# Kernel optimization log

Measured on AMD Instinct MI355X. Metric: run time of the kernel, lower is better.

## Reference

```python
import jax, jax.numpy as jnp
import numpy as np

EPS = 1e-32

def round_ste(x):
    # straight-through rounding: forward round, identity gradient
    return x + jax.lax.stop_gradient(jnp.round(x) - x)

def setup_inputs() -> dict:
    key = jax.random.key(0)
    x = jax.random.normal(key, (4096, 11008), dtype=jnp.float32)  # [out_ch, d_in]
    return {"x": x, "n_bits": 4}

def reference(x, n_bits):
    # --- find_params (per_channel=True, sym=True, method='log_2') ---
    half_levels = float(2 ** (n_bits - 1))  # number of log2 levels
    xmin = jnp.minimum(x.min(axis=1), 0.0)          # [C]
    xmax = jnp.maximum(x.max(axis=1), 0.0)          # [C]
    xmax = jnp.maximum(jnp.abs(xmin), xmax)         # symmetric range
    xmin = -xmax
    # get_code_map, branch code_no_2 >= 2^(n_bits-1): pure base-2 codes
    max_val = jnp.floor(jnp.log2(xmax + EPS) + 0.5)
    neg_max_val = jnp.floor(jnp.log2(-xmin + EPS) + 0.5)
    max_val = jnp.maximum(max_val, neg_max_val)
    zero = (max_val - half_levels + 1.0)[:, None]   # [C,1] zero point (min exponent)
    # asym_map = 0 (sym), code_map = all True -> real_code_map = 2, scale = 1 (p=1)
    # --- quantize (method='log_2', hardware_approx=False) ---
    x_log = jnp.log2(jnp.abs(x) + EPS)              # log(|x/scale|+eps)/log(2), scale=1
    x_int = round_ste(x_log)
    x_c1 = jnp.maximum(x_int - zero, -1.0)          # clamp min = -(1+asym/2)*code_map = -1
    x_c = jnp.minimum(x_c1 - half_levels, -1.0)     # clamp max = -1
    x_quant = jnp.exp2(x_c + half_levels + zero)    # pow(2, exponent)
    x_quant = jnp.where(x_c1 <= -1.0, 0.0, x_quant) # zero_flag & code_map
    s = jax.lax.stop_gradient(jnp.sign(x))          # sign(x.detach())
    return x_quant * s                              # * scale (=1)
```

## Files before the change

kernel.cpp:

```cpp
#include <hip/hip_runtime.h>
#include <math.h>


#define NROW 4096
#define D    11008
#define D4   (D / 4)
#define EPSF 1e-32f
#define NTHREADS 256

typedef float floatx4 __attribute__((ext_vector_type(4)));

__device__ __forceinline__ float quant_one(float v, float zero) {
    float a  = fabsf(v);
    float xl = log2f(a + EPSF);
    float xi = rintf(xl);
    float c1 = fmaxf(xi - zero, -1.0f);
    float c  = fminf(c1 - 8.0f, -1.0f);
    float q  = exp2f(c + 8.0f + zero);
    if (c1 <= -1.0f) q = 0.0f;
    return copysignf(q, v);
}

__global__ __launch_bounds__(NTHREADS)
void log2_quant_kernel(const float* __restrict__ x, float* __restrict__ out) {
    __shared__ float wmax[NTHREADS / 64];

    const int r   = blockIdx.x;
    const int tid = threadIdx.x;
    const floatx4* __restrict__ xr = (const floatx4*)(x + (size_t)r * D);
    floatx4* __restrict__ outr     = (floatx4*)(out + (size_t)r * D);

    float m = 0.0f;
    for (int i = tid; i < D4; i += NTHREADS) {
        floatx4 v = xr[i];
        m = fmaxf(m, fmaxf(fmaxf(fabsf(v.x), fabsf(v.y)),
                           fmaxf(fabsf(v.z), fabsf(v.w))));
    }

    #pragma unroll
    for (int off = 32; off > 0; off >>= 1)
        m = fmaxf(m, __shfl_down(m, off, 64));

    const int lane = tid & 63;
    const int wid  = tid >> 6;
    if (lane == 0) wmax[wid] = m;
    __syncthreads();

    const float xmax    = fmaxf(fmaxf(wmax[0], wmax[1]), fmaxf(wmax[2], wmax[3]));
    const float max_val = floorf(log2f(xmax + EPSF) + 0.5f);
    const float zero    = max_val - 7.0f;

    for (int i = tid; i < D4; i += NTHREADS) {
        floatx4 v = xr[i];
        floatx4 o;
        o.x = quant_one(v.x, zero);
        o.y = quant_one(v.y, zero);
        o.z = quant_one(v.z, zero);
        o.w = quant_one(v.w, zero);
        __builtin_nontemporal_store(o, &outr[i]);
    }
}

extern "C" void kernel_launch(void* const* d_in, const int* in_sizes, int n_in,
                              void* d_out, int out_size, void* d_ws, size_t ws_size,
                              hipStream_t stream) {
    const float* x = (const float*)d_in[0];
    float* out     = (float*)d_out;
    log2_quant_kernel<<<NROW, NTHREADS, 0, stream>>>(x, out);
}
```

Before: 327.3 us.

## Split row-max reduction and quantization into separate kernels with 2D grid

Replaces the single per-row kernel with a reduction kernel that writes per-row zero points to workspace, followed by an elementwise quant kernel over a tiles-by-rows grid. The reduction loop is unrolled with two independent accumulators for more memory-level parallelism. This exposes far more blocks for the bandwidth-heavy quant pass but rereads x in a separate launch, relying on cache to avoid a second full HBM read.

```diff
diff --git a/kernel.cpp b/kernel.cpp
--- a/kernel.cpp
+++ b/kernel.cpp
@@ -7,6 +7,7 @@
 #define D4   (D / 4)
 #define EPSF 1e-32f
 #define NTHREADS 256
+#define NTILES 11
 
 typedef float floatx4 __attribute__((ext_vector_type(4)));
 
@@ -22,43 +23,62 @@
 }
 
 __global__ __launch_bounds__(NTHREADS)
-void log2_quant_kernel(const float* __restrict__ x, float* __restrict__ out) {
+void rowzero_kernel(const float* __restrict__ x, float* __restrict__ zeros) {
     __shared__ float wmax[NTHREADS / 64];
 
     const int r   = blockIdx.x;
     const int tid = threadIdx.x;
     const floatx4* __restrict__ xr = (const floatx4*)(x + (size_t)r * D);
-    floatx4* __restrict__ outr     = (floatx4*)(out + (size_t)r * D);
 
-    float m = 0.0f;
-    for (int i = tid; i < D4; i += NTHREADS) {
-        floatx4 v = xr[i];
-        m = fmaxf(m, fmaxf(fmaxf(fabsf(v.x), fabsf(v.y)),
-                           fmaxf(fabsf(v.z), fabsf(v.w))));
+    float m0 = 0.0f, m1 = 0.0f;
+    int i = tid;
+    #pragma unroll
+    for (int k = 0; k < 5; ++k, i += 2 * NTHREADS) {
+        floatx4 a = xr[i];
+        floatx4 b = xr[i + NTHREADS];
+        m0 = fmaxf(m0, fmaxf(fmaxf(fabsf(a.x), fabsf(a.y)),
+                             fmaxf(fabsf(a.z), fabsf(a.w))));
+        m1 = fmaxf(m1, fmaxf(fmaxf(fabsf(b.x), fabsf(b.y)),
+                             fmaxf(fabsf(b.z), fabsf(b.w))));
     }
+    if (i < D4) {
+        floatx4 a = xr[i];
+        m0 = fmaxf(m0, fmaxf(fmaxf(fabsf(a.x), fabsf(a.y)),
+                             fmaxf(fabsf(a.z), fabsf(a.w))));
+    }
+    float m = fmaxf(m0, m1);
 
     #pragma unroll
     for (int off = 32; off > 0; off >>= 1)
         m = fmaxf(m, __shfl_down(m, off, 64));
 
-    const int lane = tid & 63;
-    const int wid  = tid >> 6;
-    if (lane == 0) wmax[wid] = m;
+    if ((tid & 63) == 0) wmax[tid >> 6] = m;
     __syncthreads();
 
-    const float xmax    = fmaxf(fmaxf(wmax[0], wmax[1]), fmaxf(wmax[2], wmax[3]));
-    const float max_val = floorf(log2f(xmax + EPSF) + 0.5f);
-    const float zero    = max_val - 7.0f;
+    if (tid == 0) {
+        float xmax = fmaxf(fmaxf(wmax[0], wmax[1]), fmaxf(wmax[2], wmax[3]));
+        zeros[r] = floorf(log2f(xmax + EPSF) + 0.5f) - 7.0f;
+    }
+}
 
-    for (int i = tid; i < D4; i += NTHREADS) {
-        floatx4 v = xr[i];
-        floatx4 o;
-        o.x = quant_one(v.x, zero);
-        o.y = quant_one(v.y, zero);
-        o.z = quant_one(v.z, zero);
-        o.w = quant_one(v.w, zero);
-        __builtin_nontemporal_store(o, &outr[i]);
-    }
+__global__ __launch_bounds__(NTHREADS)
+void quant_kernel(const float* __restrict__ x, const float* __restrict__ zeros,
+                  float* __restrict__ out) {
+    const int r = blockIdx.y;
+    const int i = blockIdx.x * NTHREADS + threadIdx.x;
+    if (i >= D4) return;
+
+    const float zero = zeros[r];
+    const floatx4* __restrict__ xr = (const floatx4*)(x + (size_t)r * D);
+    floatx4* __restrict__ outr     = (floatx4*)(out + (size_t)r * D);
+
+    floatx4 v = xr[i];
+    floatx4 o;
+    o.x = quant_one(v.x, zero);
+    o.y = quant_one(v.y, zero);
+    o.z = quant_one(v.z, zero);
+    o.w = quant_one(v.w, zero);
+    __builtin_nontemporal_store(o, &outr[i]);
 }
 
 extern "C" void kernel_launch(void* const* d_in, const int* in_sizes, int n_in,
@@ -66,5 +86,7 @@
                               hipStream_t stream) {
     const float* x = (const float*)d_in[0];
     float* out     = (float*)d_out;
-    log2_quant_kernel<<<NROW, NTHREADS, 0, stream>>>(x, out);
+    float* zeros   = (float*)d_ws;
+    rowzero_kernel<<<NROW, NTHREADS, 0, stream>>>(x, zeros);
+    quant_kernel<<<dim3(NTILES, NROW), NTHREADS, 0, stream>>>(x, zeros, out);
 }
```

Result: no change. 321.0 us (-1.9%).

## Cache each row slice in registers to avoid second global read

Applied to the files above, without the earlier changes.

Each thread now loads its whole share of the row (ten float4 vectors plus a predicated tail) into registers once. The max reduction and the quantization pass both run from those registers, so the second read of x from global memory is gone. Loops are fully unrolled and launch bounds request six blocks per CU, which raises register pressure and may limit occupancy or cause spills.

```diff
diff --git a/kernel.cpp b/kernel.cpp
--- a/kernel.cpp
+++ b/kernel.cpp
@@ -7,6 +7,8 @@
 #define D4   (D / 4)
 #define EPSF 1e-32f
 #define NTHREADS 256
+#define K_FULL 10
+#define TAIL   (D4 - K_FULL * NTHREADS)
 
 typedef float floatx4 __attribute__((ext_vector_type(4)));
 
@@ -21,43 +23,56 @@
     return copysignf(q, v);
 }
 
-__global__ __launch_bounds__(NTHREADS)
-void log2_quant_kernel(const float* __restrict__ x, float* __restrict__ out) {
+__global__ __launch_bounds__(NTHREADS, 6)
+void fused_quant_kernel(const float* __restrict__ x, float* __restrict__ out) {
     __shared__ float wmax[NTHREADS / 64];
 
     const int r   = blockIdx.x;
     const int tid = threadIdx.x;
     const floatx4* __restrict__ xr = (const floatx4*)(x + (size_t)r * D);
     floatx4* __restrict__ outr     = (floatx4*)(out + (size_t)r * D);
+    const bool has_tail = tid < TAIL;
+
+    floatx4 v[K_FULL + 1];
+    #pragma unroll
+    for (int k = 0; k < K_FULL; ++k)
+        v[k] = xr[tid + k * NTHREADS];
+    if (has_tail)
+        v[K_FULL] = xr[tid + K_FULL * NTHREADS];
+    else
+        v[K_FULL] = (floatx4)(0.0f);
 
     float m = 0.0f;
-    for (int i = tid; i < D4; i += NTHREADS) {
-        floatx4 v = xr[i];
-        m = fmaxf(m, fmaxf(fmaxf(fabsf(v.x), fabsf(v.y)),
-                           fmaxf(fabsf(v.z), fabsf(v.w))));
-    }
+    #pragma unroll
+    for (int k = 0; k <= K_FULL; ++k)
+        m = fmaxf(m, fmaxf(fmaxf(fabsf(v[k].x), fabsf(v[k].y)),
+                           fmaxf(fabsf(v[k].z), fabsf(v[k].w))));
 
     #pragma unroll
     for (int off = 32; off > 0; off >>= 1)
         m = fmaxf(m, __shfl_down(m, off, 64));
-
-    const int lane = tid & 63;
-    const int wid  = tid >> 6;
-    if (lane == 0) wmax[wid] = m;
+    if ((tid & 63) == 0) wmax[tid >> 6] = m;
     __syncthreads();
 
-    const float xmax    = fmaxf(fmaxf(wmax[0], wmax[1]), fmaxf(wmax[2], wmax[3]));
-    const float max_val = floorf(log2f(xmax + EPSF) + 0.5f);
-    const float zero    = max_val - 7.0f;
+    const float xmax = fmaxf(fmaxf(wmax[0], wmax[1]), fmaxf(wmax[2], wmax[3]));
+    const float zero = floorf(log2f(xmax + EPSF) + 0.5f) - 7.0f;
 
-    for (int i = tid; i < D4; i += NTHREADS) {
-        floatx4 v = xr[i];
+    #pragma unroll
+    for (int k = 0; k < K_FULL; ++k) {
         floatx4 o;
-        o.x = quant_one(v.x, zero);
-        o.y = quant_one(v.y, zero);
-        o.z = quant_one(v.z, zero);
-        o.w = quant_one(v.w, zero);
-        __builtin_nontemporal_store(o, &outr[i]);
+        o.x = quant_one(v[k].x, zero);
+        o.y = quant_one(v[k].y, zero);
+        o.z = quant_one(v[k].z, zero);
+        o.w = quant_one(v[k].w, zero);
+        __builtin_nontemporal_store(o, &outr[tid + k * NTHREADS]);
+    }
+    if (has_tail) {
+        floatx4 o;
+        o.x = quant_one(v[K_FULL].x, zero);
+        o.y = quant_one(v[K_FULL].y, zero);
+        o.z = quant_one(v[K_FULL].z, zero);
+        o.w = quant_one(v[K_FULL].w, zero);
+        __builtin_nontemporal_store(o, &outr[tid + K_FULL * NTHREADS]);
     }
 }
 
@@ -66,5 +81,5 @@
                               hipStream_t stream) {
     const float* x = (const float*)d_in[0];
     float* out     = (float*)d_out;
-    log2_quant_kernel<<<NROW, NTHREADS, 0, stream>>>(x, out);
+    fused_quant_kernel<<<NROW, NTHREADS, 0, stream>>>(x, out);
 }
```

Result: faster. 308.1 us (-5.9%).
